# Optimization experiments

Hardware: AMD Instinct MI355X
Metric: run time of the kernel (lower is better)

Reference implementation:

```python
import jax, jax.numpy as jnp
import numpy as np

N_NODES = 20000
NUM_DRUGS = 2048
NUM_DPI = 200000
IN_C = 256
EMB = 256
HID = 512
OUT = 1
N_CL = 8
B = 16384


def setup_inputs() -> dict:
    key = jax.random.key(0)
    ks = jax.random.split(key, 10)
    x = jax.random.normal(ks[0], (N_NODES, IN_C), jnp.float32)
    # bipartite DPI edges: drug ids in [0, NUM_DRUGS), protein ids in [NUM_DRUGS, N_NODES)
    d = jax.random.randint(ks[1], (NUM_DPI,), 0, NUM_DRUGS)
    p = jax.random.randint(ks[2], (NUM_DPI,), NUM_DRUGS, N_NODES)
    edge_index = jnp.concatenate([jnp.stack([d, p]), jnp.stack([p, d])], axis=1)  # [2, 2*NUM_DPI]
    drug_drug_batch = jax.random.randint(ks[3], (2, B), 0, NUM_DRUGS)
    edge_cell_lines = jax.random.randint(ks[4], (B,), 0, N_CL)
    Wg1 = jax.random.normal(ks[5], (IN_C, EMB), jnp.float32) / np.float32(np.sqrt(IN_C))
    bg1 = jnp.zeros((EMB,), jnp.float32)
    Wg2 = jax.random.normal(ks[6], (EMB, EMB), jnp.float32) / np.float32(np.sqrt(EMB))
    bg2 = jnp.zeros((EMB,), jnp.float32)
    W1 = jax.random.normal(ks[7], (N_CL, 2 * EMB, HID), jnp.float32) / np.float32(np.sqrt(2 * EMB))
    b1 = jnp.zeros((N_CL, HID), jnp.float32)
    W2 = jax.random.normal(ks[8], (N_CL, HID, OUT), jnp.float32) / np.float32(np.sqrt(HID))
    b2 = jnp.zeros((N_CL, OUT), jnp.float32)
    return dict(x=x, edge_index=edge_index, drug_drug_batch=drug_drug_batch,
                edge_cell_lines=edge_cell_lines, num_drugs=NUM_DRUGS,
                Wg1=Wg1, bg1=bg1, Wg2=Wg2, bg2=bg2, W1=W1, b1=b1, W2=W2, b2=b2)


def _gcn(h_in, row, col, W, b, n):
    # PyG GCNConv: self-loops already appended to (row, col); symmetric normalization.
    h = h_in @ W  # [N, EMB]
    deg = jax.ops.segment_sum(jnp.ones(col.shape[0], h.dtype), col, num_segments=n)
    dinv = jnp.where(deg > 0, jax.lax.rsqrt(jnp.maximum(deg, 1e-12)), 0.0)
    msg = h[row] * (dinv[row] * dinv[col])[:, None]
    return jax.ops.segment_sum(msg, col, num_segments=n) + b


def reference(x, edge_index, drug_drug_batch, edge_cell_lines, num_drugs,
              Wg1, bg1, Wg2, bg2, W1, b1, W2, b2):
    n = x.shape[0]
    ar = jnp.arange(n, dtype=edge_index.dtype)
    row = jnp.concatenate([edge_index[0], ar])
    col = jnp.concatenate([edge_index[1], ar])
    h = jax.nn.relu(_gcn(x, row, col, Wg1, bg1, n))
    h = jax.nn.relu(_gcn(h, row, col, Wg2, bg2, n))
    # scatter-mean pool node embeddings of proteins into per-drug graph embeddings
    num_dpi = edge_index.shape[1] // 2
    avg = jnp.sort(edge_index[:, :num_dpi], axis=0)  # row0=drug id, row1=protein id
    node_emb = h[avg[1]]  # [NUM_DPI, EMB]
    sums = jax.ops.segment_sum(node_emb, avg[0], num_segments=num_drugs)
    cnt = jax.ops.segment_sum(jnp.ones(num_dpi, h.dtype), avg[0], num_segments=num_drugs)
    graph = sums / jnp.maximum(cnt, 1.0)[:, None]  # [NUM_DRUGS, EMB]
    xcat = jnp.concatenate([graph[drug_drug_batch[0]], graph[drug_drug_batch[1]]], axis=1)  # [B, 2*EMB]
    # per-cell-line MLP routing: run each expert over all rows, then gather per-row expert output
    n_cl = W1.shape[0]
    outs = jnp.stack([jax.nn.relu(xcat @ W1[c] + b1[c]) @ W2[c] + b2[c] for c in range(n_cl)])  # [C, B, OUT]
    preds = outs[edge_cell_lines, jnp.arange(xcat.shape[0])]  # [B, OUT]
    return preds
```

## Files before the change

kernel.cpp:

```cpp
#include <hip/hip_runtime.h>
#include <hip/hip_bf16.h>

#define N_NODES 20000
#define NUM_DRUGS 2048
#define N_PROT (N_NODES - NUM_DRUGS)
#define NUM_DPI 200000
#define E2 400000
#define CDIM 256
#define HID 512
#define N_CL 8
#define BATCH 16384
#define HN 8192

#define STRD 32
#define STRP 16
#define ELLD 192
#define ELLP 48

#define NB_FILL 782
#define NB_T64 512
#define NB_TWG 32
#define NB_SPLIT 20000

#define MT_NODE 313
#define NB_GNODE 640

#define NB_AGG_D NUM_DRUGS
#define NB_AGG_P ((N_PROT + 3) / 4)

typedef __attribute__((ext_vector_type(8))) short short8;
typedef __attribute__((ext_vector_type(4))) float floatx4;

__device__ inline unsigned short f2bf(float f) {
    unsigned u = __float_as_uint(f);
    u += 0x7fff + ((u >> 16) & 1);
    return (unsigned short)(u >> 16);
}
__device__ inline float bf2f(unsigned short h) {
    return __uint_as_float((unsigned)h << 16);
}
__device__ inline void gload16(const void* g, void* l) {
    __builtin_amdgcn_global_load_lds(
        (const __attribute__((address_space(1))) void*)g,
        (__attribute__((address_space(3))) void*)l, 16, 0, 0);
}
__device__ inline float4 f4fma(float4 v, float s, float4 a) {
    a.x = fmaf(v.x, s, a.x); a.y = fmaf(v.y, s, a.y);
    a.z = fmaf(v.z, s, a.z); a.w = fmaf(v.w, s, a.w);
    return a;
}
__device__ inline float4 bf4(const unsigned short* p) {
    ushort4 q = *(const ushort4*)p;
    return make_float4(bf2f(q.x), bf2f(q.y), bf2f(q.z), bf2f(q.w));
}

__global__ void zero_counts(int* cur_d, int* cur_p) {
    int i = blockIdx.x * blockDim.x + threadIdx.x;
    if (i < N_NODES) cur_p[i * STRP] = 0;
    if (i < NUM_DRUGS) cur_d[i * STRD] = 0;
}

__global__ __launch_bounds__(256) void prep_all(
        const int* __restrict__ ei, int* __restrict__ cur_d,
        int* __restrict__ adj_drug, int* __restrict__ cur_p,
        int* __restrict__ adj_prot,
        const float* __restrict__ x, unsigned short* __restrict__ xbf,
        const float* __restrict__ Wg1, const float* __restrict__ Wg2,
        unsigned short* __restrict__ wg1Tb, unsigned short* __restrict__ wg2Tb,
        const float* __restrict__ W1, unsigned short* __restrict__ W1Tb) {
    __shared__ float ld[64 * 65];
    int b = blockIdx.x;
    int t = threadIdx.x;
    int tx = t & 63, ty = t >> 6;
    if (b < NB_FILL) {
        int e = b * 256 + t;
        if (e < NUM_DPI) {
            int d = ei[e];
            int p = ei[E2 + e];
            int posd = atomicAdd(&cur_d[d * STRD], 1);
            int posp = atomicAdd(&cur_p[p * STRP], 1);
            if (posd < ELLD) adj_drug[d * ELLD + posd] = p;
            if (posp < ELLP) adj_prot[(size_t)p * ELLP + posp] = d;
        }
        return;
    }
    b -= NB_FILL;
    if (b < NB_T64) {
        int m = b >> 5;
        int k0 = (b & 3) * 64, n0 = ((b >> 2) & 7) * 64;
        const float* Wm = W1 + (size_t)m * CDIM * HID;
#pragma unroll
        for (int rr = 0; rr < 16; rr++) {
            int kl = rr * 4 + ty;
            ld[tx * 65 + kl] = Wm[(size_t)(k0 + kl) * HID + n0 + tx];
        }
        __syncthreads();
        size_t obase = (size_t)m * HID * CDIM;
#pragma unroll
        for (int rr = 0; rr < 16; rr++) {
            int nl = rr * 4 + ty;
            size_t o = obase + (size_t)(n0 + nl) * CDIM + k0 + tx;
            W1Tb[o] = f2bf(ld[nl * 65 + tx]);
        }
        return;
    }
    b -= NB_T64;
    if (b < NB_TWG) {
        const float* W = (b >> 4) ? Wg2 : Wg1;
        unsigned short* ob = (b >> 4) ? wg2Tb : wg1Tb;
        int k0 = (b & 3) * 64, n0 = ((b >> 2) & 3) * 64;
#pragma unroll
        for (int rr = 0; rr < 16; rr++) {
            int kl = rr * 4 + ty;
            ld[tx * 65 + kl] = W[(size_t)(k0 + kl) * CDIM + n0 + tx];
        }
        __syncthreads();
#pragma unroll
        for (int rr = 0; rr < 16; rr++) {
            int nl = rr * 4 + ty;
            size_t o = (size_t)(n0 + nl) * CDIM + k0 + tx;
            ob[o] = f2bf(ld[nl * 65 + tx]);
        }
        return;
    }
    b -= NB_TWG;
    {
        int i = b * 256 + t;
        xbf[i] = f2bf(x[i]);
    }
}

template <int BM, int BN, int SWZ>
__global__ __launch_bounds__(256) void gemm_mfma(
        const unsigned short* __restrict__ A,
        const unsigned short* __restrict__ BT,
        unsigned short* __restrict__ Cbf,
        int M, int K, int N, int mTiles,
        const int* __restrict__ cur_d, const int* __restrict__ cur_p,
        float* __restrict__ dinv) {
    if ((int)blockIdx.x >= mTiles) {
        int i = (((int)blockIdx.x - mTiles) * (int)gridDim.y + (int)blockIdx.y) * 256
                + (int)threadIdx.x;
        if (i < N_NODES) {
            int deg = (i < NUM_DRUGS) ? cur_d[i * STRD] : cur_p[i * STRP];
            dinv[i] = rsqrtf((float)(deg + 1));
        }
        return;
    }
    constexpr int MI = BM / 32;
    constexpr int NJ = BN / 32;
    __shared__ unsigned short sA[2][BM * 32];
    __shared__ unsigned short sB[2][BN * 32];
    int t = threadIdx.x;
    int wv = t >> 6, lane = t & 63, quad = lane >> 4, l15 = lane & 15;
    int bx = blockIdx.x, by = blockIdx.y;
    if constexpr (SWZ == 1) {
        int w = by * 16 + bx;
        int xcd = w & 7, j = w >> 3;
        bx = j & 15;
        by = xcd * 8 + (j >> 4);
    }
    if constexpr (SWZ == 2) {
        int id = bx;
        int xcd = id & 7, k = id >> 3;
        by = k & 1;
        bx = xcd * 40 + (k >> 1);
        if (bx >= MT_NODE) return;
    }
    int m0 = bx * BM, n0 = by * BN;
    int m0w = (wv >> 1) * (BM / 2), n0w = (wv & 1) * (BN / 2);
    floatx4 zero = {0.f, 0.f, 0.f, 0.f};
    floatx4 acc[MI][NJ];
#pragma unroll
    for (int i = 0; i < MI; i++)
#pragma unroll
        for (int j = 0; j < NJ; j++) acc[i][j] = zero;

    auto STAGE = [&](int buf, int kk) {
#pragma unroll
        for (int s = t; s < BM * 4; s += 256) {
            int row = s >> 2, pos = s & 3;
            int ch = pos ^ ((row >> 1) & 3);
            int arow = m0 + row; if (arow > M - 1) arow = M - 1;
            gload16(A + (size_t)arow * K + kk + ch * 8, &sA[buf][s * 8]);
        }
#pragma unroll
        for (int s = t; s < BN * 4; s += 256) {
            int row = s >> 2, pos = s & 3;
            int ch = pos ^ ((row >> 1) & 3);
            int brow = n0 + row; if (brow > N - 1) brow = N - 1;
            gload16(BT + (size_t)brow * K + kk + ch * 8, &sB[buf][s * 8]);
        }
    };

    int nk = K >> 5;
    STAGE(0, 0);
    asm volatile("s_waitcnt vmcnt(0)" ::: "memory");
    __builtin_amdgcn_s_barrier();
    int cur = 0;
    for (int it = 0; it < nk; ++it) {
        if (it + 1 < nk) STAGE(cur ^ 1, (it + 1) << 5);
        short8 af[MI], bf[NJ];
        int posq = quad ^ ((l15 >> 1) & 3);
#pragma unroll
        for (int i = 0; i < MI; i++) {
            int sl = (m0w + i * 16 + l15) * 4 + posq;
            af[i] = *(const short8*)&sA[cur][sl * 8];
        }
#pragma unroll
        for (int j = 0; j < NJ; j++) {
            int sl = (n0w + j * 16 + l15) * 4 + posq;
            bf[j] = *(const short8*)&sB[cur][sl * 8];
        }
#pragma unroll
        for (int i = 0; i < MI; i++)
#pragma unroll
            for (int j = 0; j < NJ; j++)
                acc[i][j] = __builtin_amdgcn_mfma_f32_16x16x32_bf16(af[i], bf[j], acc[i][j], 0, 0, 0);
        if (it + 1 < nk) {
            asm volatile("s_waitcnt vmcnt(0)" ::: "memory");
            __builtin_amdgcn_s_barrier();
            cur ^= 1;
        }
    }
#pragma unroll
    for (int i = 0; i < MI; i++) {
        int gr = m0 + m0w + i * 16 + quad * 4;
#pragma unroll
        for (int r = 0; r < 4; r++) {
            if (gr + r < M) {
#pragma unroll
                for (int j = 0; j < NJ; j++) {
                    size_t o = (size_t)(gr + r) * N + n0 + n0w + j * 16 + l15;
                    Cbf[o] = f2bf(acc[i][j][r]);
                }
            }
        }
    }
}

__global__ __launch_bounds__(256) void aggregate1(const unsigned short* __restrict__ tmpbf,
                                                  const int* __restrict__ cur_d,
                                                  const int* __restrict__ adj_drug,
                                                  const int* __restrict__ cur_p,
                                                  const int* __restrict__ adj_prot,
                                                  const float* __restrict__ dinv,
                                                  const float* __restrict__ bias,
                                                  unsigned short* __restrict__ outbf) {
    __shared__ float4 red[4][64];
    int b = blockIdx.x;
    int lane = threadIdx.x & 63;
    if (b < NB_AGG_D) {
        int d = b;
        int w = threadIdx.x >> 6;
        const int* adj = adj_drug + (size_t)d * ELLD;
        int ecnt = cur_d[d * STRD];
        int e = ecnt < ELLD ? ecnt : ELLD;
        float4 a0 = make_float4(0.f, 0.f, 0.f, 0.f);
        float4 a1 = a0, a2 = a0, a3 = a0;
        int idx = w;
        for (; idx + 12 < e; idx += 16) {
            int j0 = adj[idx], j1 = adj[idx + 4], j2 = adj[idx + 8], j3 = adj[idx + 12];
            float d0 = dinv[j0], d1 = dinv[j1], d2 = dinv[j2], d3 = dinv[j3];
            float4 v0 = bf4(&tmpbf[(size_t)j0 * CDIM + lane * 4]);
            float4 v1 = bf4(&tmpbf[(size_t)j1 * CDIM + lane * 4]);
            float4 v2 = bf4(&tmpbf[(size_t)j2 * CDIM + lane * 4]);
            float4 v3 = bf4(&tmpbf[(size_t)j3 * CDIM + lane * 4]);
            a0 = f4fma(v0, d0, a0);
            a1 = f4fma(v1, d1, a1);
            a2 = f4fma(v2, d2, a2);
            a3 = f4fma(v3, d3, a3);
        }
        for (; idx < e; idx += 4) {
            int j = adj[idx];
            a0 = f4fma(bf4(&tmpbf[(size_t)j * CDIM + lane * 4]), dinv[j], a0);
        }
        a0.x = (a0.x + a1.x) + (a2.x + a3.x);
        a0.y = (a0.y + a1.y) + (a2.y + a3.y);
        a0.z = (a0.z + a1.z) + (a2.z + a3.z);
        a0.w = (a0.w + a1.w) + (a2.w + a3.w);
        red[w][lane] = a0;
        __syncthreads();
        if (w == 0) {
            float di = dinv[d];
            float4 r0 = red[0][lane], r1 = red[1][lane], r2 = red[2][lane], r3 = red[3][lane];
            float4 self = bf4(&tmpbf[(size_t)d * CDIM + lane * 4]);
            float4 acc;
            acc.x = (r0.x + r1.x) + (r2.x + r3.x) + self.x * di;
            acc.y = (r0.y + r1.y) + (r2.y + r3.y) + self.y * di;
            acc.z = (r0.z + r1.z) + (r2.z + r3.z) + self.z * di;
            acc.w = (r0.w + r1.w) + (r2.w + r3.w) + self.w * di;
            float4 bv = ((const float4*)bias)[lane];
            ushort4 o;
            o.x = f2bf(fmaxf(fmaf(acc.x, di, bv.x), 0.f));
            o.y = f2bf(fmaxf(fmaf(acc.y, di, bv.y), 0.f));
            o.z = f2bf(fmaxf(fmaf(acc.z, di, bv.z), 0.f));
            o.w = f2bf(fmaxf(fmaf(acc.w, di, bv.w), 0.f));
            *(ushort4*)&outbf[(size_t)d * CDIM + lane * 4] = o;
        }
        return;
    }
    int i = NUM_DRUGS + (b - NB_AGG_D) * 4 + (threadIdx.x >> 6);
    if (i >= N_NODES) return;
    float di = dinv[i];
    float4 a0 = make_float4(0.f, 0.f, 0.f, 0.f);
    float4 a1 = a0, a2 = a0, a3 = a0;
    const int* adj = adj_prot + (size_t)i * ELLP;
    int e = cur_p[i * STRP];
    int idx = 0;
    for (; idx + 4 <= e; idx += 4) {
        int j0 = adj[idx + 0], j1 = adj[idx + 1];
        int j2 = adj[idx + 2], j3 = adj[idx + 3];
        float d0 = dinv[j0], d1 = dinv[j1], d2 = dinv[j2], d3 = dinv[j3];
        float4 v0 = bf4(&tmpbf[(size_t)j0 * CDIM + lane * 4]);
        float4 v1 = bf4(&tmpbf[(size_t)j1 * CDIM + lane * 4]);
        float4 v2 = bf4(&tmpbf[(size_t)j2 * CDIM + lane * 4]);
        float4 v3 = bf4(&tmpbf[(size_t)j3 * CDIM + lane * 4]);
        a0 = f4fma(v0, d0, a0);
        a1 = f4fma(v1, d1, a1);
        a2 = f4fma(v2, d2, a2);
        a3 = f4fma(v3, d3, a3);
    }
    for (; idx < e; idx++) {
        int j = adj[idx];
        a0 = f4fma(bf4(&tmpbf[(size_t)j * CDIM + lane * 4]), dinv[j], a0);
    }
    float4 self = bf4(&tmpbf[(size_t)i * CDIM + lane * 4]);
    float4 acc;
    acc.x = (a0.x + a1.x) + (a2.x + a3.x) + self.x * di;
    acc.y = (a0.y + a1.y) + (a2.y + a3.y) + self.y * di;
    acc.z = (a0.z + a1.z) + (a2.z + a3.z) + self.z * di;
    acc.w = (a0.w + a1.w) + (a2.w + a3.w) + self.w * di;
    float4 bv = ((const float4*)bias)[lane];
    ushort4 o;
    o.x = f2bf(fmaxf(fmaf(acc.x, di, bv.x), 0.f));
    o.y = f2bf(fmaxf(fmaf(acc.y, di, bv.y), 0.f));
    o.z = f2bf(fmaxf(fmaf(acc.z, di, bv.z), 0.f));
    o.w = f2bf(fmaxf(fmaf(acc.w, di, bv.w), 0.f));
    *(ushort4*)&outbf[(size_t)i * CDIM + lane * 4] = o;
}

__global__ __launch_bounds__(256) void aggregate2p(const unsigned short* __restrict__ t2bf,
                                                   const int* __restrict__ cur_p,
                                                   const int* __restrict__ adj_prot,
                                                   const float* __restrict__ dinv,
                                                   const float* __restrict__ bias,
                                                   unsigned short* __restrict__ h2bf) {
    int w = (blockIdx.x * blockDim.x + threadIdx.x) >> 6;
    int lane = threadIdx.x & 63;
    if (w >= N_PROT) return;
    int i = NUM_DRUGS + w;
    float di = dinv[i];
    float4 a0 = make_float4(0.f, 0.f, 0.f, 0.f);
    float4 a1 = a0, a2 = a0, a3 = a0;
    const int* adj = adj_prot + (size_t)i * ELLP;
    int e = cur_p[i * STRP];
    int idx = 0;
    for (; idx + 4 <= e; idx += 4) {
        int j0 = adj[idx + 0], j1 = adj[idx + 1];
        int j2 = adj[idx + 2], j3 = adj[idx + 3];
        float d0 = dinv[j0], d1 = dinv[j1], d2 = dinv[j2], d3 = dinv[j3];
        float4 v0 = bf4(&t2bf[(size_t)j0 * CDIM + lane * 4]);
        float4 v1 = bf4(&t2bf[(size_t)j1 * CDIM + lane * 4]);
        float4 v2 = bf4(&t2bf[(size_t)j2 * CDIM + lane * 4]);
        float4 v3 = bf4(&t2bf[(size_t)j3 * CDIM + lane * 4]);
        a0 = f4fma(v0, d0, a0);
        a1 = f4fma(v1, d1, a1);
        a2 = f4fma(v2, d2, a2);
        a3 = f4fma(v3, d3, a3);
    }
    for (; idx < e; idx++) {
        int j = adj[idx];
        a0 = f4fma(bf4(&t2bf[(size_t)j * CDIM + lane * 4]), dinv[j], a0);
    }
    float4 self = bf4(&t2bf[(size_t)i * CDIM + lane * 4]);
    float4 acc;
    acc.x = (a0.x + a1.x) + (a2.x + a3.x) + self.x * di;
    acc.y = (a0.y + a1.y) + (a2.y + a3.y) + self.y * di;
    acc.z = (a0.z + a1.z) + (a2.z + a3.z) + self.z * di;
    acc.w = (a0.w + a1.w) + (a2.w + a3.w) + self.w * di;
    float4 bv = ((const float4*)bias)[lane];
    ushort4 o;
    o.x = f2bf(fmaxf(fmaf(acc.x, di, bv.x), 0.f));
    o.y = f2bf(fmaxf(fmaf(acc.y, di, bv.y), 0.f));
    o.z = f2bf(fmaxf(fmaf(acc.z, di, bv.z), 0.f));
    o.w = f2bf(fmaxf(fmaf(acc.w, di, bv.w), 0.f));
    *(ushort4*)&h2bf[(size_t)i * CDIM + lane * 4] = o;
}

__global__ __launch_bounds__(256) void pool_drugs(const unsigned short* __restrict__ h2bf,
                                                  unsigned short* __restrict__ Gb,
                                                  const int* __restrict__ cur_d,
                                                  const int* __restrict__ adj_drug) {
    __shared__ float4 red[4][64];
    int d = blockIdx.x;
    int w = threadIdx.x >> 6, lane = threadIdx.x & 63;
    const int* adj = adj_drug + (size_t)d * ELLD;
    int ecnt = cur_d[d * STRD];
    int e = ecnt < ELLD ? ecnt : ELLD;
    float4 a0 = make_float4(0.f, 0.f, 0.f, 0.f);
    float4 a1 = a0, a2 = a0, a3 = a0;
    int idx = w;
    for (; idx + 12 < e; idx += 16) {
        int j0 = adj[idx], j1 = adj[idx + 4], j2 = adj[idx + 8], j3 = adj[idx + 12];
        float4 v0 = bf4(&h2bf[(size_t)j0 * CDIM + lane * 4]);
        float4 v1 = bf4(&h2bf[(size_t)j1 * CDIM + lane * 4]);
        float4 v2 = bf4(&h2bf[(size_t)j2 * CDIM + lane * 4]);
        float4 v3 = bf4(&h2bf[(size_t)j3 * CDIM + lane * 4]);
        a0.x += v0.x; a0.y += v0.y; a0.z += v0.z; a0.w += v0.w;
        a1.x += v1.x; a1.y += v1.y; a1.z += v1.z; a1.w += v1.w;
        a2.x += v2.x; a2.y += v2.y; a2.z += v2.z; a2.w += v2.w;
        a3.x += v3.x; a3.y += v3.y; a3.z += v3.z; a3.w += v3.w;
    }
    for (; idx < e; idx += 4) {
        float4 v = bf4(&h2bf[(size_t)adj[idx] * CDIM + lane * 4]);
        a0.x += v.x; a0.y += v.y; a0.z += v.z; a0.w += v.w;
    }
    a0.x = (a0.x + a1.x) + (a2.x + a3.x);
    a0.y = (a0.y + a1.y) + (a2.y + a3.y);
    a0.z = (a0.z + a1.z) + (a2.z + a3.z);
    a0.w = (a0.w + a1.w) + (a2.w + a3.w);
    red[w][lane] = a0;
    __syncthreads();
    if (w == 0) {
        float4 r0 = red[0][lane], r1 = red[1][lane], r2 = red[2][lane], r3 = red[3][lane];
        float4 acc;
        acc.x = (r0.x + r1.x) + (r2.x + r3.x);
        acc.y = (r0.y + r1.y) + (r2.y + r3.y);
        acc.z = (r0.z + r1.z) + (r2.z + r3.z);
        acc.w = (r0.w + r1.w) + (r2.w + r3.w);
        float sc = 1.f / (float)(ecnt > 1 ? ecnt : 1);
        ushort4 o;
        o.x = f2bf(acc.x * sc);
        o.y = f2bf(acc.y * sc);
        o.z = f2bf(acc.z * sc);
        o.w = f2bf(acc.w * sc);
        *(ushort4*)&Gb[(size_t)d * CDIM + lane * 4] = o;
    }
}

__global__ __launch_bounds__(256) void mlp_out(const unsigned short* __restrict__ Hbf,
                                               const int* __restrict__ ddb,
                                               const int* __restrict__ ecl,
                                               const float* __restrict__ b1,
                                               const float* __restrict__ W2,
                                               const float* __restrict__ b2,
                                               float* __restrict__ outp) {
    int r = (blockIdx.x * blockDim.x + threadIdx.x) >> 6;
    int lane = threadIdx.x & 63;
    if (r >= BATCH) return;
    int c = ecl[r];
    int d0 = ddb[r], d1 = ddb[BATCH + r];
    int n = lane * 8;
    const unsigned short* h0 = Hbf + (size_t)d0 * HN + (size_t)(c * 2) * HID + n;
    const unsigned short* h1 = Hbf + (size_t)d1 * HN + (size_t)(c * 2 + 1) * HID + n;
    const float* b1e = b1 + (size_t)c * HID + n;
    const float* w2e = W2 + (size_t)c * HID + n;
    short8 a8 = *(const short8*)h0;
    short8 b8 = *(const short8*)h1;
    float4 bb0 = *(const float4*)(b1e);
    float4 bb1 = *(const float4*)(b1e + 4);
    float4 w0 = *(const float4*)(w2e);
    float4 w1 = *(const float4*)(w2e + 4);
    float s = 0.f;
    float h;
    h = bf2f((unsigned short)a8[0]) + bf2f((unsigned short)b8[0]) + bb0.x;
    s = fmaf(fmaxf(h, 0.f), w0.x, s);
    h = bf2f((unsigned short)a8[1]) + bf2f((unsigned short)b8[1]) + bb0.y;
    s = fmaf(fmaxf(h, 0.f), w0.y, s);
    h = bf2f((unsigned short)a8[2]) + bf2f((unsigned short)b8[2]) + bb0.z;
    s = fmaf(fmaxf(h, 0.f), w0.z, s);
    h = bf2f((unsigned short)a8[3]) + bf2f((unsigned short)b8[3]) + bb0.w;
    s = fmaf(fmaxf(h, 0.f), w0.w, s);
    h = bf2f((unsigned short)a8[4]) + bf2f((unsigned short)b8[4]) + bb1.x;
    s = fmaf(fmaxf(h, 0.f), w1.x, s);
    h = bf2f((unsigned short)a8[5]) + bf2f((unsigned short)b8[5]) + bb1.y;
    s = fmaf(fmaxf(h, 0.f), w1.y, s);
    h = bf2f((unsigned short)a8[6]) + bf2f((unsigned short)b8[6]) + bb1.z;
    s = fmaf(fmaxf(h, 0.f), w1.z, s);
    h = bf2f((unsigned short)a8[7]) + bf2f((unsigned short)b8[7]) + bb1.w;
    s = fmaf(fmaxf(h, 0.f), w1.w, s);
    s += __shfl_xor(s, 1);
    s += __shfl_xor(s, 2);
    s += __shfl_xor(s, 4);
    s += __shfl_xor(s, 8);
    s += __shfl_xor(s, 16);
    s += __shfl_xor(s, 32);
    if (lane == 0) outp[r] = s + b2[c];
}

extern "C" void kernel_launch(void* const* d_in, const int* in_sizes, int n_in,
                              void* d_out, int out_size, void* d_ws, size_t ws_size,
                              hipStream_t stream) {
    const float* x   = (const float*)d_in[0];
    const int* ei    = (const int*)d_in[1];
    const int* ddb   = (const int*)d_in[2];
    const int* ecl   = (const int*)d_in[3];
    const float* Wg1 = (const float*)d_in[5];
    const float* bg1 = (const float*)d_in[6];
    const float* Wg2 = (const float*)d_in[7];
    const float* bg2 = (const float*)d_in[8];
    const float* W1  = (const float*)d_in[9];
    const float* b1  = (const float*)d_in[10];
    const float* W2  = (const float*)d_in[11];
    const float* b2  = (const float*)d_in[12];
    float* outp = (float*)d_out;

    const size_t HRES = (size_t)NUM_DRUGS * HN * sizeof(float);
    char* r0 = (char*)d_ws;
    unsigned short* Hbf   = (unsigned short*)d_ws;
    unsigned short* t2bf  = (unsigned short*)r0;
    unsigned short* t1bf  = (unsigned short*)(r0 + 20480000);
    unsigned short* h2bf  = t1bf;
    unsigned short* h1bf  = (unsigned short*)(r0 + 30720000);
    unsigned short* xbf   = h1bf;
    char* p = r0 + 51200000;
    auto alloc = [&](size_t bytes) {
        char* r = p;
        p += (bytes + 255) & ~size_t(255);
        return (void*)r;
    };
    float* dinv    = (float*)alloc(sizeof(float) * N_NODES);
    int* cur_d     = (int*)alloc(sizeof(int) * NUM_DRUGS * STRD);
    int* cur_p     = (int*)alloc(sizeof(int) * N_NODES * STRP);
    int* adj_drug  = (int*)alloc(sizeof(int) * NUM_DRUGS * ELLD);
    int* adj_prot  = (int*)alloc(sizeof(int) * (size_t)N_NODES * ELLP);
    p = (char*)d_ws + ((HRES + 255) & ~size_t(255));
    unsigned short* Gb    = (unsigned short*)alloc(2 * NUM_DRUGS * CDIM);
    unsigned short* wg1Tb = (unsigned short*)alloc(2 * CDIM * CDIM);
    unsigned short* wg2Tb = (unsigned short*)alloc(2 * CDIM * CDIM);
    unsigned short* W1Tb  = (unsigned short*)alloc(2 * (size_t)N_CL * HID * HID);

    zero_counts<<<(N_NODES + 255) / 256, 256, 0, stream>>>(cur_d, cur_p);
    prep_all<<<NB_FILL + NB_T64 + NB_TWG + NB_SPLIT, 256, 0, stream>>>(
        ei, cur_d, adj_drug, cur_p, adj_prot,
        x, xbf, Wg1, Wg2, wg1Tb, wg2Tb, W1, W1Tb);
    gemm_mfma<64, 128, 2><<<dim3(NB_GNODE + 79, 1), 256, 0, stream>>>(
        xbf, wg1Tb, t1bf, N_NODES, CDIM, CDIM,
        NB_GNODE, cur_d, cur_p, dinv);
    aggregate1<<<NB_AGG_D + NB_AGG_P, 256, 0, stream>>>(
        t1bf, cur_d, adj_drug, cur_p, adj_prot, dinv, bg1, h1bf);
    gemm_mfma<64, 128, 2><<<dim3(NB_GNODE, 1), 256, 0, stream>>>(
        h1bf, wg2Tb, t2bf, N_NODES, CDIM, CDIM,
        NB_GNODE, nullptr, nullptr, nullptr);
    aggregate2p<<<(N_PROT * 64 + 255) / 256, 256, 0, stream>>>(
        t2bf, cur_p, adj_prot, dinv, bg2, h2bf);
    pool_drugs<<<NUM_DRUGS, 256, 0, stream>>>(h2bf, Gb, cur_d, adj_drug);
    gemm_mfma<128, 128, 1><<<dim3(NUM_DRUGS / 128, HN / 128), 256, 0, stream>>>(
        Gb, W1Tb, Hbf, NUM_DRUGS, CDIM, HN,
        NUM_DRUGS / 128, nullptr, nullptr, nullptr);
    mlp_out<<<(BATCH * 64) / 256, 256, 0, stream>>>(Hbf, ddb, ecl, b1, W2, b2, outp);
}
```

Baseline: 215.8 us.

## Fuse per-cell-line MLP into bucketed gathered GEMM, dropping the full hidden precompute

Rows are bucketed by cell line with an atomic counter in the prep kernel. A new fused kernel gathers the two drug embeddings per row straight into shared memory and runs an MFMA GEMM against that cell line's W1 slab. It then applies bias, ReLU and the W2 dot product in the epilogue. This replaces the precompute of all-drug × all-expert hidden activations and the separate gather kernel, avoiding a large intermediate write and re-read. The tile count per cell line is fixed, so a very unbalanced cell-line distribution could overflow the tiles, and the grid is small relative to the GPU.

Measured after the change: 260.0 us. +20.5%, slower.

```diff
diff --git a/kernel.cpp b/kernel.cpp
--- a/kernel.cpp
+++ b/kernel.cpp
@@ -10,14 +10,15 @@
 #define HID 512
 #define N_CL 8
 #define BATCH 16384
-#define HN 8192
 
 #define STRD 32
 #define STRP 16
+#define STRB 16
 #define ELLD 192
 #define ELLP 48
 
 #define NB_FILL 782
+#define NB_BKT 64
 #define NB_T64 512
 #define NB_TWG 32
 #define NB_SPLIT 20000
@@ -27,6 +28,8 @@
 
 #define NB_AGG_D NUM_DRUGS
 #define NB_AGG_P ((N_PROT + 3) / 4)
+
+#define MLP_TILES 44
 
 typedef __attribute__((ext_vector_type(8))) short short8;
 typedef __attribute__((ext_vector_type(4))) float floatx4;
@@ -54,16 +57,19 @@
     return make_float4(bf2f(q.x), bf2f(q.y), bf2f(q.z), bf2f(q.w));
 }
 
-__global__ void zero_counts(int* cur_d, int* cur_p) {
+__global__ void zero_counts(int* cur_d, int* cur_p, int* bcnt) {
     int i = blockIdx.x * blockDim.x + threadIdx.x;
     if (i < N_NODES) cur_p[i * STRP] = 0;
     if (i < NUM_DRUGS) cur_d[i * STRD] = 0;
+    if (i < N_CL) bcnt[i * STRB] = 0;
 }
 
 __global__ __launch_bounds__(256) void prep_all(
         const int* __restrict__ ei, int* __restrict__ cur_d,
         int* __restrict__ adj_drug, int* __restrict__ cur_p,
         int* __restrict__ adj_prot,
+        const int* __restrict__ ecl, int* __restrict__ bcnt,
+        int* __restrict__ bidx,
         const float* __restrict__ x, unsigned short* __restrict__ xbf,
         const float* __restrict__ Wg1, const float* __restrict__ Wg2,
         unsigned short* __restrict__ wg1Tb, unsigned short* __restrict__ wg2Tb,
@@ -85,6 +91,14 @@
         return;
     }
     b -= NB_FILL;
+    if (b < NB_BKT) {
+        int r = b * 256 + t;
+        int c = ecl[r];
+        int pos = atomicAdd(&bcnt[c * STRB], 1);
+        bidx[c * BATCH + pos] = r;
+        return;
+    }
+    b -= NB_BKT;
     if (b < NB_T64) {
         int m = b >> 5;
         int k0 = (b & 3) * 64, n0 = ((b >> 2) & 7) * 64;
@@ -154,12 +168,6 @@
     int t = threadIdx.x;
     int wv = t >> 6, lane = t & 63, quad = lane >> 4, l15 = lane & 15;
     int bx = blockIdx.x, by = blockIdx.y;
-    if constexpr (SWZ == 1) {
-        int w = by * 16 + bx;
-        int xcd = w & 7, j = w >> 3;
-        bx = j & 15;
-        by = xcd * 8 + (j >> 4);
-    }
     if constexpr (SWZ == 2) {
         int id = bx;
         int xcd = id & 7, k = id >> 3;
@@ -236,6 +244,131 @@
                 }
             }
         }
+    }
+}
+
+__global__ __launch_bounds__(256) void mlp_fused(
+        const unsigned short* __restrict__ Gb,
+        const unsigned short* __restrict__ W1Tb,
+        const int* __restrict__ bcnt, const int* __restrict__ bidx,
+        const int* __restrict__ ddb,
+        const float* __restrict__ b1, const float* __restrict__ W2,
+        const float* __restrict__ b2, float* __restrict__ outp) {
+    constexpr int BM = 64, BN = 128, MI = 2, NJ = 4;
+    __shared__ unsigned short sA[2][BM * 32];
+    __shared__ unsigned short sB[2][BN * 32];
+    __shared__ float b1s[BN], w2s[BN];
+    __shared__ int rowsLds[BM];
+    __shared__ int drgA[BM], drgB[BM];
+    __shared__ float red[4][BM];
+    int c = blockIdx.y;
+    int tile = blockIdx.x;
+    int cnt = bcnt[c * STRB];
+    int m0 = tile * BM;
+    if (m0 >= cnt) return;
+    int t = threadIdx.x;
+    int wv = t >> 6, lane = t & 63, quad = lane >> 4, l15 = lane & 15;
+    if (t < BM) {
+        int slot = m0 + t;
+        int slotc = slot < cnt ? slot : cnt - 1;
+        int r = bidx[c * BATCH + slotc];
+        rowsLds[t] = (slot < cnt) ? r : -1;
+        drgA[t] = ddb[r];
+        drgB[t] = ddb[BATCH + r];
+    }
+    __syncthreads();
+    int arow = t >> 2;
+    int chA = (t & 3) ^ ((t >> 3) & 3);
+    int dA0 = drgA[arow], dA1 = drgB[arow];
+    int m0w = (wv >> 1) * (BM / 2), n0w = (wv & 1) * (BN / 2);
+    const size_t slabBase = ((size_t)c * 2) * HID * CDIM;
+    float rowAcc = 0.f;
+    floatx4 zero = {0.f, 0.f, 0.f, 0.f};
+    constexpr int nk = (2 * CDIM) >> 5;
+
+    for (int pass = 0; pass < 4; ++pass) {
+        int n0 = pass * BN;
+        if (t < BN) {
+            b1s[t] = b1[(size_t)c * HID + n0 + t];
+            w2s[t] = W2[(size_t)c * HID + n0 + t];
+        }
+        floatx4 acc[MI][NJ];
+#pragma unroll
+        for (int i = 0; i < MI; i++)
+#pragma unroll
+            for (int j = 0; j < NJ; j++) acc[i][j] = zero;
+
+        auto STAGE = [&](int buf, int kk) {
+            int half = kk >> 8;
+            int kl = kk & 255;
+            int drug = half ? dA1 : dA0;
+            gload16(Gb + (size_t)drug * CDIM + kl + chA * 8, &sA[buf][t * 8]);
+            const unsigned short* Wb = W1Tb + slabBase + (size_t)half * HID * CDIM;
+#pragma unroll
+            for (int s = t; s < BN * 4; s += 256) {
+                int row = s >> 2, pos = s & 3;
+                int ch = pos ^ ((row >> 1) & 3);
+                gload16(Wb + (size_t)(n0 + row) * CDIM + kl + ch * 8, &sB[buf][s * 8]);
+            }
+        };
+
+        __syncthreads();
+        STAGE(0, 0);
+        asm volatile("s_waitcnt vmcnt(0)" ::: "memory");
+        __builtin_amdgcn_s_barrier();
+        int cur = 0;
+        for (int it = 0; it < nk; ++it) {
+            if (it + 1 < nk) STAGE(cur ^ 1, (it + 1) << 5);
+            short8 af[MI], bf[NJ];
+            int posq = quad ^ ((l15 >> 1) & 3);
+#pragma unroll
+            for (int i = 0; i < MI; i++) {
+                int sl = (m0w + i * 16 + l15) * 4 + posq;
+                af[i] = *(const short8*)&sA[cur][sl * 8];
+            }
+#pragma unroll
+            for (int j = 0; j < NJ; j++) {
+                int sl = (n0w + j * 16 + l15) * 4 + posq;
+                bf[j] = *(const short8*)&sB[cur][sl * 8];
+            }
+#pragma unroll
+            for (int i = 0; i < MI; i++)
+#pragma unroll
+                for (int j = 0; j < NJ; j++)
+                    acc[i][j] = __builtin_amdgcn_mfma_f32_16x16x32_bf16(af[i], bf[j], acc[i][j], 0, 0, 0);
+            if (it + 1 < nk) {
+                asm volatile("s_waitcnt vmcnt(0)" ::: "memory");
+                __builtin_amdgcn_s_barrier();
+                cur ^= 1;
+            }
+        }
+#pragma unroll
+        for (int i = 0; i < MI; i++) {
+#pragma unroll
+            for (int r = 0; r < 4; r++) {
+                float p = 0.f;
+#pragma unroll
+                for (int j = 0; j < NJ; j++) {
+                    int col = n0w + j * 16 + l15;
+                    float z = acc[i][j][r] + b1s[col];
+                    p = fmaf(fmaxf(z, 0.f), w2s[col], p);
+                }
+                p += __shfl_xor(p, 1);
+                p += __shfl_xor(p, 2);
+                p += __shfl_xor(p, 4);
+                p += __shfl_xor(p, 8);
+                if (l15 == 0) red[wv][m0w + i * 16 + quad * 4 + r] = p;
+            }
+        }
+        __syncthreads();
+        if (t < BM) {
+            int rh = t >> 5;
+            rowAcc += red[rh * 2][t] + red[rh * 2 + 1][t];
+        }
+    }
+    if (t < BM) {
+        int r = rowsLds[t];
+        if (r >= 0) outp[r] = rowAcc + b2[c];
     }
 }
 
@@ -439,56 +572,6 @@
     }
 }
 
-__global__ __launch_bounds__(256) void mlp_out(const unsigned short* __restrict__ Hbf,
-                                               const int* __restrict__ ddb,
-                                               const int* __restrict__ ecl,
-                                               const float* __restrict__ b1,
-                                               const float* __restrict__ W2,
-                                               const float* __restrict__ b2,
-                                               float* __restrict__ outp) {
-    int r = (blockIdx.x * blockDim.x + threadIdx.x) >> 6;
-    int lane = threadIdx.x & 63;
-    if (r >= BATCH) return;
-    int c = ecl[r];
-    int d0 = ddb[r], d1 = ddb[BATCH + r];
-    int n = lane * 8;
-    const unsigned short* h0 = Hbf + (size_t)d0 * HN + (size_t)(c * 2) * HID + n;
-    const unsigned short* h1 = Hbf + (size_t)d1 * HN + (size_t)(c * 2 + 1) * HID + n;
-    const float* b1e = b1 + (size_t)c * HID + n;
-    const float* w2e = W2 + (size_t)c * HID + n;
-    short8 a8 = *(const short8*)h0;
-    short8 b8 = *(const short8*)h1;
-    float4 bb0 = *(const float4*)(b1e);
-    float4 bb1 = *(const float4*)(b1e + 4);
-    float4 w0 = *(const float4*)(w2e);
-    float4 w1 = *(const float4*)(w2e + 4);
-    float s = 0.f;
-    float h;
-    h = bf2f((unsigned short)a8[0]) + bf2f((unsigned short)b8[0]) + bb0.x;
-    s = fmaf(fmaxf(h, 0.f), w0.x, s);
-    h = bf2f((unsigned short)a8[1]) + bf2f((unsigned short)b8[1]) + bb0.y;
-    s = fmaf(fmaxf(h, 0.f), w0.y, s);
-    h = bf2f((unsigned short)a8[2]) + bf2f((unsigned short)b8[2]) + bb0.z;
-    s = fmaf(fmaxf(h, 0.f), w0.z, s);
-    h = bf2f((unsigned short)a8[3]) + bf2f((unsigned short)b8[3]) + bb0.w;
-    s = fmaf(fmaxf(h, 0.f), w0.w, s);
-    h = bf2f((unsigned short)a8[4]) + bf2f((unsigned short)b8[4]) + bb1.x;
-    s = fmaf(fmaxf(h, 0.f), w1.x, s);
-    h = bf2f((unsigned short)a8[5]) + bf2f((unsigned short)b8[5]) + bb1.y;
-    s = fmaf(fmaxf(h, 0.f), w1.y, s);
-    h = bf2f((unsigned short)a8[6]) + bf2f((unsigned short)b8[6]) + bb1.z;
-    s = fmaf(fmaxf(h, 0.f), w1.z, s);
-    h = bf2f((unsigned short)a8[7]) + bf2f((unsigned short)b8[7]) + bb1.w;
-    s = fmaf(fmaxf(h, 0.f), w1.w, s);
-    s += __shfl_xor(s, 1);
-    s += __shfl_xor(s, 2);
-    s += __shfl_xor(s, 4);
-    s += __shfl_xor(s, 8);
-    s += __shfl_xor(s, 16);
-    s += __shfl_xor(s, 32);
-    if (lane == 0) outp[r] = s + b2[c];
-}
-
 extern "C" void kernel_launch(void* const* d_in, const int* in_sizes, int n_in,
                               void* d_out, int out_size, void* d_ws, size_t ws_size,
                               hipStream_t stream) {
@@ -506,9 +589,7 @@
     const float* b2  = (const float*)d_in[12];
     float* outp = (float*)d_out;
 
-    const size_t HRES = (size_t)NUM_DRUGS * HN * sizeof(float);
     char* r0 = (char*)d_ws;
-    unsigned short* Hbf   = (unsigned short*)d_ws;
     unsigned short* t2bf  = (unsigned short*)r0;
     unsigned short* t1bf  = (unsigned short*)(r0 + 20480000);
     unsigned short* h2bf  = t1bf;
@@ -525,15 +606,16 @@
     int* cur_p     = (int*)alloc(sizeof(int) * N_NODES * STRP);
     int* adj_drug  = (int*)alloc(sizeof(int) * NUM_DRUGS * ELLD);
     int* adj_prot  = (int*)alloc(sizeof(int) * (size_t)N_NODES * ELLP);
-    p = (char*)d_ws + ((HRES + 255) & ~size_t(255));
+    int* bcnt      = (int*)alloc(sizeof(int) * N_CL * STRB);
+    int* bidx      = (int*)alloc(sizeof(int) * (size_t)N_CL * BATCH);
     unsigned short* Gb    = (unsigned short*)alloc(2 * NUM_DRUGS * CDIM);
     unsigned short* wg1Tb = (unsigned short*)alloc(2 * CDIM * CDIM);
     unsigned short* wg2Tb = (unsigned short*)alloc(2 * CDIM * CDIM);
     unsigned short* W1Tb  = (unsigned short*)alloc(2 * (size_t)N_CL * HID * HID);
 
-    zero_counts<<<(N_NODES + 255) / 256, 256, 0, stream>>>(cur_d, cur_p);
-    prep_all<<<NB_FILL + NB_T64 + NB_TWG + NB_SPLIT, 256, 0, stream>>>(
-        ei, cur_d, adj_drug, cur_p, adj_prot,
+    zero_counts<<<(N_NODES + 255) / 256, 256, 0, stream>>>(cur_d, cur_p, bcnt);
+    prep_all<<<NB_FILL + NB_BKT + NB_T64 + NB_TWG + NB_SPLIT, 256, 0, stream>>>(
+        ei, cur_d, adj_drug, cur_p, adj_prot, ecl, bcnt, bidx,
         x, xbf, Wg1, Wg2, wg1Tb, wg2Tb, W1, W1Tb);
     gemm_mfma<64, 128, 2><<<dim3(NB_GNODE + 79, 1), 256, 0, stream>>>(
         xbf, wg1Tb, t1bf, N_NODES, CDIM, CDIM,
@@ -546,8 +628,6 @@
     aggregate2p<<<(N_PROT * 64 + 255) / 256, 256, 0, stream>>>(
         t2bf, cur_p, adj_prot, dinv, bg2, h2bf);
     pool_drugs<<<NUM_DRUGS, 256, 0, stream>>>(h2bf, Gb, cur_d, adj_drug);
-    gemm_mfma<128, 128, 1><<<dim3(NUM_DRUGS / 128, HN / 128), 256, 0, stream>>>(
-        Gb, W1Tb, Hbf, NUM_DRUGS, CDIM, HN,
-        NUM_DRUGS / 128, nullptr, nullptr, nullptr);
-    mlp_out<<<(BATCH * 64) / 256, 256, 0, stream>>>(Hbf, ddb, ecl, b1, W2, b2, outp);
-}
+    mlp_fused<<<dim3(MLP_TILES, N_CL), 256, 0, stream>>>(
+        Gb, W1Tb, bcnt, bidx, ddb, b1, W2, b2, outp);
+}
```
